# Kernel tuning notes

Measured on AMD Instinct MI355X. Metric: run time of the kernel, lower is better.

Reference implementation:

```python
import jax, jax.numpy as jnp
import numpy as np

B, F = 16384, 2048


def setup_inputs() -> dict:
    key = jax.random.key(0)
    k0, k1 = jax.random.split(key)
    x0 = jax.random.normal(k0, (B, F), dtype=jnp.float32)
    x = jax.random.normal(k1, (B, F), dtype=jnp.float32)
    # Parameters as initialized by the torch module
    weights = jnp.ones((F,), dtype=jnp.float32)
    bias = jnp.zeros((F,), dtype=jnp.float32)
    return {"x0": x0, "x": x, "weights": weights, "bias": bias}


def reference(x0, x, weights, bias):
    # torch: bmm(x0[:, :, None], x[:, None, :]) @ weights + bias + x
    # The [B,F,F] outer product contracted with weights over the last axis
    # equals x0 * (x . weights), computed in O(B*F) without the F^2 tensor.
    xw = jnp.einsum('bf,f->b', x, weights)  # [B]
    return x0 * xw[:, None] + bias + x
```

## Files before the change

kernel.cpp:

```cpp
#include <hip/hip_runtime.h>


#define F_DIM 2048

__global__ __launch_bounds__(256) void cross_row_kernel(
    const float* __restrict__ x0,
    const float* __restrict__ x,
    const float* __restrict__ w,
    const float* __restrict__ bias,
    float* __restrict__ out)
{
    const int b = blockIdx.x;
    const int t = threadIdx.x;
    const long long row = (long long)b * F_DIM;

    const float4* __restrict__ x4  = (const float4*)(x  + row);
    const float4* __restrict__ x04 = (const float4*)(x0 + row);
    const float4* __restrict__ w4  = (const float4*)w;
    const float4* __restrict__ bi4 = (const float4*)bias;
    float4* __restrict__ o4 = (float4*)(out + row);

    float4 xa = x4[t];
    float4 xb = x4[t + 256];
    float4 wa = w4[t];
    float4 wb = w4[t + 256];

    float4 x0a = x04[t];
    float4 x0b = x04[t + 256];
    float4 ba  = bi4[t];
    float4 bb  = bi4[t + 256];

    float partial = xa.x * wa.x + xa.y * wa.y + xa.z * wa.z + xa.w * wa.w
                  + xb.x * wb.x + xb.y * wb.y + xb.z * wb.z + xb.w * wb.w;

    #pragma unroll
    for (int off = 32; off > 0; off >>= 1)
        partial += __shfl_down(partial, off, 64);

    __shared__ float sdot[4];
    __shared__ float dot_s;
    const int wave = t >> 6;
    const int lane = t & 63;
    if (lane == 0) sdot[wave] = partial;
    __syncthreads();
    if (t == 0) dot_s = sdot[0] + sdot[1] + sdot[2] + sdot[3];
    __syncthreads();
    const float dot = dot_s;

    float4 oa, ob;
    oa.x = x0a.x * dot + ba.x + xa.x;
    oa.y = x0a.y * dot + ba.y + xa.y;
    oa.z = x0a.z * dot + ba.z + xa.z;
    oa.w = x0a.w * dot + ba.w + xa.w;
    ob.x = x0b.x * dot + bb.x + xb.x;
    ob.y = x0b.y * dot + bb.y + xb.y;
    ob.z = x0b.z * dot + bb.z + xb.z;
    ob.w = x0b.w * dot + bb.w + xb.w;

    o4[t]       = oa;
    o4[t + 256] = ob;
}

extern "C" void kernel_launch(void* const* d_in, const int* in_sizes, int n_in,
                              void* d_out, int out_size, void* d_ws, size_t ws_size,
                              hipStream_t stream) {
    const float* x0   = (const float*)d_in[0];
    const float* x    = (const float*)d_in[1];
    const float* w    = (const float*)d_in[2];
    const float* bias = (const float*)d_in[3];
    float* out = (float*)d_out;

    const int B = in_sizes[0] / F_DIM;
    cross_row_kernel<<<B, 256, 0, stream>>>(x0, x, w, bias, out);
}
```

Measured before the change: 303.5 us.

## Map one row per wavefront to drop block-level reduction barriers

Each 64-lane wavefront now handles a whole row, with 8 float4 loads per lane, so the dot product is reduced entirely with xor shuffles. Shared memory and both __syncthreads are gone, and four rows are processed per 256-thread block. This trades barrier overhead for much higher register use per lane (24+ float4 live), which may lower occupancy. It also assumes B is a multiple of 4.

New measurement: 313.6 us. +3.3%, slower.

```diff
diff --git a/kernel.cpp b/kernel.cpp
--- a/kernel.cpp
+++ b/kernel.cpp
@@ -2,16 +2,19 @@
 
 
 #define F_DIM 2048
+#define PER_LANE 8
 
-__global__ __launch_bounds__(256) void cross_row_kernel(
+__global__ __launch_bounds__(256) void cross_wave_kernel(
     const float* __restrict__ x0,
     const float* __restrict__ x,
     const float* __restrict__ w,
     const float* __restrict__ bias,
     float* __restrict__ out)
 {
-    const int b = blockIdx.x;
-    const int t = threadIdx.x;
+    const int t    = threadIdx.x;
+    const int wave = t >> 6;
+    const int lane = t & 63;
+    const int b    = blockIdx.x * 4 + wave;
     const long long row = (long long)b * F_DIM;
 
     const float4* __restrict__ x4  = (const float4*)(x  + row);
@@ -20,45 +23,36 @@
     const float4* __restrict__ bi4 = (const float4*)bias;
     float4* __restrict__ o4 = (float4*)(out + row);
 
-    float4 xa = x4[t];
-    float4 xb = x4[t + 256];
-    float4 wa = w4[t];
-    float4 wb = w4[t + 256];
-
-    float4 x0a = x04[t];
-    float4 x0b = x04[t + 256];
-    float4 ba  = bi4[t];
-    float4 bb  = bi4[t + 256];
-
-    float partial = xa.x * wa.x + xa.y * wa.y + xa.z * wa.z + xa.w * wa.w
-                  + xb.x * wb.x + xb.y * wb.y + xb.z * wb.z + xb.w * wb.w;
+    float4 xv[PER_LANE], x0v[PER_LANE], wv[PER_LANE];
 
     #pragma unroll
-    for (int off = 32; off > 0; off >>= 1)
-        partial += __shfl_down(partial, off, 64);
+    for (int i = 0; i < PER_LANE; ++i) xv[i] = x4[lane + 64 * i];
+    #pragma unroll
+    for (int i = 0; i < PER_LANE; ++i) wv[i] = w4[lane + 64 * i];
+    #pragma unroll
+    for (int i = 0; i < PER_LANE; ++i) x0v[i] = x04[lane + 64 * i];
 
-    __shared__ float sdot[4];
-    __shared__ float dot_s;
-    const int wave = t >> 6;
-    const int lane = t & 63;
-    if (lane == 0) sdot[wave] = partial;
-    __syncthreads();
-    if (t == 0) dot_s = sdot[0] + sdot[1] + sdot[2] + sdot[3];
-    __syncthreads();
-    const float dot = dot_s;
+    float partial = 0.f;
+    #pragma unroll
+    for (int i = 0; i < PER_LANE; ++i) {
+        partial += xv[i].x * wv[i].x + xv[i].y * wv[i].y
+                 + xv[i].z * wv[i].z + xv[i].w * wv[i].w;
+    }
 
-    float4 oa, ob;
-    oa.x = x0a.x * dot + ba.x + xa.x;
-    oa.y = x0a.y * dot + ba.y + xa.y;
-    oa.z = x0a.z * dot + ba.z + xa.z;
-    oa.w = x0a.w * dot + ba.w + xa.w;
-    ob.x = x0b.x * dot + bb.x + xb.x;
-    ob.y = x0b.y * dot + bb.y + xb.y;
-    ob.z = x0b.z * dot + bb.z + xb.z;
-    ob.w = x0b.w * dot + bb.w + xb.w;
+    #pragma unroll
+    for (int off = 1; off < 64; off <<= 1)
+        partial += __shfl_xor(partial, off, 64);
 
-    o4[t]       = oa;
-    o4[t + 256] = ob;
+    #pragma unroll
+    for (int i = 0; i < PER_LANE; ++i) {
+        float4 bv = bi4[lane + 64 * i];
+        float4 o;
+        o.x = x0v[i].x * partial + bv.x + xv[i].x;
+        o.y = x0v[i].y * partial + bv.y + xv[i].y;
+        o.z = x0v[i].z * partial + bv.z + xv[i].z;
+        o.w = x0v[i].w * partial + bv.w + xv[i].w;
+        o4[lane + 64 * i] = o;
+    }
 }
 
 extern "C" void kernel_launch(void* const* d_in, const int* in_sizes, int n_in,
@@ -71,5 +65,5 @@
     float* out = (float*)d_out;
 
     const int B = in_sizes[0] / F_DIM;
-    cross_row_kernel<<<B, 256, 0, stream>>>(x0, x, w, bias, out);
+    cross_wave_kernel<<<B / 4, 256, 0, stream>>>(x0, x, w, bias, out);
 }
```
